# Optimization experiments

Measured on AMD Instinct MI355X. Metric: run time of the kernel, lower is better.

Reference implementation:

```python
import jax, jax.numpy as jnp
import numpy as np
import math

B, L, D, H, FACTOR = 4, 2048, 256, 8, 5
DH = D // H

def setup_inputs() -> dict:
    key = jax.random.key(0)
    ks = jax.random.split(key, 12)
    s = 1.0 / math.sqrt(D)
    return {
        "q": jax.random.normal(ks[0], (B, L, D), jnp.float32),
        "k": jax.random.normal(ks[1], (B, L, D), jnp.float32),
        "v": jax.random.normal(ks[2], (B, L, D), jnp.float32),
        "Wq": jax.random.normal(ks[3], (D, D), jnp.float32) * s,
        "bq": jax.random.normal(ks[4], (D,), jnp.float32) * s,
        "Wk": jax.random.normal(ks[5], (D, D), jnp.float32) * s,
        "bk": jax.random.normal(ks[6], (D,), jnp.float32) * s,
        "Wv": jax.random.normal(ks[7], (D, D), jnp.float32) * s,
        "bv": jax.random.normal(ks[8], (D,), jnp.float32) * s,
        "Wc": jax.random.normal(ks[9], (D, D), jnp.float32) * s,
        "bc": jax.random.normal(ks[10], (D,), jnp.float32) * s,
        "index_sample": jax.random.randint(ks[11], (L,), 0, L),  # U_part = min(5*L*ceil(log1p(L)), L) = L
    }

def reference(q, k, v, Wq, bq, Wk, bk, Wv, bv, Wc, bc, index_sample):
    # projections (torch Linear: x @ W^T + b)
    qp = q @ Wq.T + bq
    kp = k @ Wk.T + bk
    vp = v @ Wv.T + bv
    # NOTE: original reshapes q with a raw view (no transpose), k/v via split()
    q4 = qp.reshape(B, H, L, DH)                       # faithful to q.view(B, H, L, dh)
    k4 = kp.reshape(B, L, H, DH).transpose(0, 2, 1, 3)
    v4 = vp.reshape(B, L, H, DH).transpose(0, 2, 1, 3)
    qf = q4.reshape(B * H, L, DH)
    kf = k4.reshape(B * H, L, DH)
    vf = v4.reshape(B * H, L, DH)
    # random K sampling (with replacement); U_part == L here
    K_sample = kf[:, index_sample, :]                  # [BH, L, dh]
    QK = jnp.einsum('bld,bud->blu', qf, K_sample)      # [BH, L, L]
    M = QK.max(axis=-1) - QK.sum(axis=-1) / L          # sparsity measure [BH, L]
    u = min(FACTOR * math.ceil(math.log1p(L)), L)      # = 40
    _, top_idx = jax.lax.top_k(-M, u)                  # topk(..., largest=False)
    Q_red = jnp.take_along_axis(qf, top_idx[:, :, None], axis=1)  # [BH, u, dh]
    scores = jnp.einsum('bud,bld->bul', Q_red, kf) / math.sqrt(DH)
    probs = jax.nn.softmax(scores, axis=-1)
    out = jnp.einsum('bul,bld->bud', probs, vf)        # [BH, u, dh]
    out = out.reshape(B, H, u, DH).transpose(0, 2, 1, 3).reshape(B, u, D)
    return out @ Wc.T + bc
```

## Files before the change

kernel.cpp:

```cpp
#include <hip/hip_runtime.h>
#include <math.h>

#define B_ 4
#define L_ 2048
#define D_ 256
#define H_ 8
#define DH_ 32
#define NH_ 32
#define U_ 40
#define LD_ 524288
#define NCH_ 16

typedef __attribute__((ext_vector_type(8))) short short8;
typedef __attribute__((ext_vector_type(4))) float floatx4;

static __device__ __forceinline__ unsigned long long ullmin_(unsigned long long a, unsigned long long b) {
    return a < b ? a : b;
}
static __device__ __forceinline__ unsigned short f2bf_rne(float x) {
    unsigned u = __float_as_uint(x);
    unsigned r = u + 0x7FFFu + ((u >> 16) & 1u);
    return (unsigned short)(r >> 16);
}
static __device__ __forceinline__ float bf2f(unsigned short h) {
    return __uint_as_float(((unsigned)h) << 16);
}

__global__ __launch_bounds__(256) void wsplit(const float* __restrict__ Wq,
                                              const float* __restrict__ Wk,
                                              const float* __restrict__ Wv,
                                              unsigned short* __restrict__ Whs,
                                              unsigned short* __restrict__ Wms,
                                              unsigned short* __restrict__ Wls) {
    const int g = blockIdx.x * 256 + threadIdx.x;
    const int mat = g >> 14;
    const int rem = g & 16383;
    const int col = rem >> 6;
    const int k4 = rem & 63;
    const float* W = (mat == 0) ? Wq : (mat == 1) ? Wk : Wv;
    const float4 x = *(const float4*)(W + (size_t)col * 256 + k4 * 4);
    float xs[4] = {x.x, x.y, x.z, x.w};
    unsigned short hv[4], mv[4], lv[4];
#pragma unroll
    for (int j = 0; j < 4; ++j) {
        hv[j] = f2bf_rne(xs[j]);
        const float e1 = xs[j] - bf2f(hv[j]);
        mv[j] = f2bf_rne(e1);
        const float e2 = e1 - bf2f(mv[j]);
        lv[j] = f2bf_rne(e2);
    }
    const int colblk = col >> 6, c64 = col & 63;
    const int nt = c64 >> 4, cin = c64 & 15;
    const int kt = k4 >> 3, kin = (k4 & 7) * 4;
    const size_t o = ((((size_t)mat * 4 + colblk) * 8 + kt) << 11) + nt * 512 + cin * 32 + kin;
    *(ushort4*)(Whs + o) = make_ushort4(hv[0], hv[1], hv[2], hv[3]);
    *(ushort4*)(Wms + o) = make_ushort4(mv[0], mv[1], mv[2], mv[3]);
    *(ushort4*)(Wls + o) = make_ushort4(lv[0], lv[1], lv[2], lv[3]);
}

__global__ __launch_bounds__(256) void gemm_proj(const float* __restrict__ q,
                                                 const float* __restrict__ k,
                                                 const float* __restrict__ v,
                                                 const unsigned short* __restrict__ Whs,
                                                 const unsigned short* __restrict__ Wms,
                                                 const unsigned short* __restrict__ Wls,
                                                 const float* __restrict__ bq,
                                                 const float* __restrict__ bk,
                                                 const float* __restrict__ bv,
                                                 float* __restrict__ qp,
                                                 float* __restrict__ kp,
                                                 float* __restrict__ vp) {
    const int mat = blockIdx.z;
    const float* X = (mat == 0) ? q : (mat == 1) ? k : v;
    const float* bias = (mat == 0) ? bq : (mat == 1) ? bk : bv;
    float* Y = (mat == 0) ? qp : (mat == 1) ? kp : vp;
    const bool vmat = (mat == 2);

    const int t = threadIdx.x;
    const int w = t >> 6, lane = t & 63;
    const int lq = lane & 15, quad = lane >> 4;
    const int rowBase = blockIdx.x * 64 + w * 16;
    const int colBase = blockIdx.y * 128;
    const int fo = lq * 32 + quad * 8;

    floatx4 acc[8];
#pragma unroll
    for (int nt2 = 0; nt2 < 8; ++nt2) acc[nt2] = (floatx4){0.f, 0.f, 0.f, 0.f};

#pragma unroll 2
    for (int kt = 0; kt < 8; ++kt) {
        short8 Ah, Am, Al;
        {
            const float* xr = X + (size_t)(rowBase + lq) * 256 + kt * 32 + quad * 8;
            const float4 x0 = *(const float4*)xr;
            const float4 x1 = *(const float4*)(xr + 4);
            float xs[8] = {x0.x, x0.y, x0.z, x0.w, x1.x, x1.y, x1.z, x1.w};
#pragma unroll
            for (int j = 0; j < 8; ++j) {
                const unsigned short h = f2bf_rne(xs[j]);
                const float e1 = xs[j] - bf2f(h);
                const unsigned short md = f2bf_rne(e1);
                Ah[j] = (short)h;
                Am[j] = (short)md;
                if (!vmat) {
                    const float e2 = e1 - bf2f(md);
                    Al[j] = (short)f2bf_rne(e2);
                }
            }
        }
#pragma unroll
        for (int nt2 = 0; nt2 < 8; ++nt2) {
            const int colblk = (blockIdx.y << 1) | (nt2 >> 2);
            const size_t pb = ((((size_t)mat * 4 + colblk) * 8 + kt) << 11) + (nt2 & 3) * 512 + fo;
            const short8 Bh = *(const short8*)(Whs + pb);
            const short8 Bm = *(const short8*)(Wms + pb);
            floatx4 a = acc[nt2];
            if (!vmat) {
                const short8 Bl = *(const short8*)(Wls + pb);
                a = __builtin_amdgcn_mfma_f32_16x16x32_bf16(Am, Bm, a, 0, 0, 0);
                a = __builtin_amdgcn_mfma_f32_16x16x32_bf16(Ah, Bl, a, 0, 0, 0);
                a = __builtin_amdgcn_mfma_f32_16x16x32_bf16(Al, Bh, a, 0, 0, 0);
                a = __builtin_amdgcn_mfma_f32_16x16x32_bf16(Ah, Bm, a, 0, 0, 0);
                a = __builtin_amdgcn_mfma_f32_16x16x32_bf16(Am, Bh, a, 0, 0, 0);
                a = __builtin_amdgcn_mfma_f32_16x16x32_bf16(Ah, Bh, a, 0, 0, 0);
            } else {
                a = __builtin_amdgcn_mfma_f32_16x16x32_bf16(Ah, Bm, a, 0, 0, 0);
                a = __builtin_amdgcn_mfma_f32_16x16x32_bf16(Am, Bh, a, 0, 0, 0);
                a = __builtin_amdgcn_mfma_f32_16x16x32_bf16(Ah, Bh, a, 0, 0, 0);
            }
            acc[nt2] = a;
        }
    }

#pragma unroll
    for (int nt2 = 0; nt2 < 8; ++nt2) {
        const int c = colBase + nt2 * 16 + lq;
        const float bv_ = bias[c];
#pragma unroll
        for (int r = 0; r < 4; ++r) {
            const int mr = rowBase + quad * 4 + r;
            Y[(size_t)mr * 256 + c] = acc[nt2][r] + bv_;
        }
    }
}

__global__ __launch_bounds__(256) void kconv_ksum(const float* __restrict__ kp,
                                                  const int* __restrict__ idx,
                                                  unsigned short* __restrict__ Khi,
                                                  unsigned short* __restrict__ Klo,
                                                  float* __restrict__ Ksum32) {
    const int blk = blockIdx.x;
    const int i = blk >> 5, uc = blk & 31;
    const int b = i >> 3, h = i & 7;
    const int t = threadIdx.x;
    const int dq = (t & 7) * 4;
    const int ur = t >> 3;

    __shared__ float part[32][36];
    float ksum[4] = {0.f, 0.f, 0.f, 0.f};

#pragma unroll
    for (int p = 0; p < 2; ++p) {
        int u = uc * 64 + p * 32 + ur;
        const float4 x = *(const float4*)(kp + (size_t)b * LD_ + (size_t)idx[u] * D_ + h * DH_ + dq);
        float xs[4] = {x.x, x.y, x.z, x.w};
        unsigned short hv[4], lv[4];
#pragma unroll
        for (int j = 0; j < 4; ++j) {
            ksum[j] += xs[j];
            hv[j] = f2bf_rne(xs[j]);
            lv[j] = f2bf_rne(xs[j] - bf2f(hv[j]));
        }
        size_t o = ((size_t)i * 2048 + u) * 32 + dq;
        *(ushort4*)(Khi + o) = make_ushort4(hv[0], hv[1], hv[2], hv[3]);
        *(ushort4*)(Klo + o) = make_ushort4(lv[0], lv[1], lv[2], lv[3]);
    }
#pragma unroll
    for (int j = 0; j < 4; ++j) part[ur][dq + j] = ksum[j];
    __syncthreads();
    if (t < 32) {
        float s = 0.f;
#pragma unroll 8
        for (int u2 = 0; u2 < 32; ++u2) s += part[u2][t];
        Ksum32[(size_t)blk * 32 + t] = s;
    }
}

__global__ __launch_bounds__(256) void mpart_mfma(const float* __restrict__ qp,
                                                  const unsigned short* __restrict__ Khi,
                                                  const unsigned short* __restrict__ Klo,
                                                  const float* __restrict__ Ksum32,
                                                  float* __restrict__ Mv,
                                                  float* __restrict__ Qmean) {
    const int blk = blockIdx.x;
    const int i = blk >> 5;
    const int lg = blk & 31;
    const int t = threadIdx.x;
    const int w = t >> 6;
    const int lane = t & 63;
    const int lq = lane & 15;
    const int quad = lane >> 4;

    __shared__ float ssum[32];
    __shared__ float red[4][64];
    if (t < 32) {
        float s = 0.f;
#pragma unroll 8
        for (int uc = 0; uc < 32; ++uc) s += Ksum32[((size_t)i * 32 + uc) * 32 + t];
        ssum[t] = s;
    }

    short8 Ah[4], Al[4];
#pragma unroll
    for (int lt = 0; lt < 4; ++lt) {
        const int l = lg * 64 + lt * 16 + lq;
        const float* qrow = qp + ((size_t)i * 2048 + l) * 32 + quad * 8;
        float4 x0 = *(const float4*)(qrow);
        float4 x1 = *(const float4*)(qrow + 4);
        float xs[8] = {x0.x, x0.y, x0.z, x0.w, x1.x, x1.y, x1.z, x1.w};
#pragma unroll
        for (int j = 0; j < 8; ++j) {
            unsigned short h = f2bf_rne(xs[j]);
            unsigned short lo = f2bf_rne(xs[j] - bf2f(h));
            Ah[lt][j] = (short)h;
            Al[lt][j] = (short)lo;
        }
    }

    floatx4 rmax[4];
#pragma unroll
    for (int lt = 0; lt < 4; ++lt)
        rmax[lt] = (floatx4){-INFINITY, -INFINITY, -INFINITY, -INFINITY};

    const size_t kfrag = ((size_t)i * 2048 + w * 512 + lq) * 32 + quad * 8;
    const unsigned short* ph = Khi + kfrag;
    const unsigned short* pl = Klo + kfrag;
#pragma unroll 2
    for (int s = 0; s < 32; ++s) {
        short8 Bh = *(const short8*)(ph + (size_t)s * 512);
        short8 Bl = *(const short8*)(pl + (size_t)s * 512);
#pragma unroll
        for (int lt = 0; lt < 4; ++lt) {
            floatx4 acc = (floatx4){0.f, 0.f, 0.f, 0.f};
            acc = __builtin_amdgcn_mfma_f32_16x16x32_bf16(Al[lt], Bh, acc, 0, 0, 0);
            acc = __builtin_amdgcn_mfma_f32_16x16x32_bf16(Ah[lt], Bl, acc, 0, 0, 0);
            acc = __builtin_amdgcn_mfma_f32_16x16x32_bf16(Ah[lt], Bh, acc, 0, 0, 0);
#pragma unroll
            for (int r = 0; r < 4; ++r) rmax[lt][r] = fmaxf(rmax[lt][r], acc[r]);
        }
    }

#pragma unroll
    for (int lt = 0; lt < 4; ++lt)
#pragma unroll
        for (int r = 0; r < 4; ++r) {
            float v = rmax[lt][r];
#pragma unroll
            for (int off = 1; off < 16; off <<= 1)
                v = fmaxf(v, __shfl_xor(v, off, 64));
            rmax[lt][r] = v;
        }
    if (lq == 0) {
#pragma unroll
        for (int lt = 0; lt < 4; ++lt)
#pragma unroll
            for (int r = 0; r < 4; ++r)
                red[w][lt * 16 + quad * 4 + r] = rmax[lt][r];
    }
    __syncthreads();
    if (t < 64) {
        const int l = lg * 64 + t;
        float m = fmaxf(fmaxf(red[0][t], red[1][t]), fmaxf(red[2][t], red[3][t]));
        const float4* q4 = (const float4*)(qp + ((size_t)i * 2048 + l) * 32);
        const float4* s4 = (const float4*)ssum;
        float qs = 0.f;
#pragma unroll
        for (int z = 0; z < 8; ++z) {
            float4 a = q4[z];
            float4 c = s4[z];
            qs = fmaf(a.x, c.x, qs);
            qs = fmaf(a.y, c.y, qs);
            qs = fmaf(a.z, c.z, qs);
            qs = fmaf(a.w, c.w, qs);
        }
        const float qm = qs * (1.0f / 2048.0f);
        Qmean[(size_t)i * 2048 + l] = qm;
        Mv[(size_t)i * 2048 + l] = m - qm;
    }
}

__global__ __launch_bounds__(256) void topk64_fast(const float* __restrict__ Mv,
                                                   int* __restrict__ candIdx) {
    const int i = blockIdx.x;
    const int t = threadIdx.x;
    const int w = t >> 6, lane = t & 63;

    __shared__ unsigned hist[256];
    __shared__ unsigned sh_prefix, sh_selBelow;
    __shared__ unsigned cnt;
    __shared__ int candLds[64];
    __shared__ unsigned long long wred[4];

    unsigned v[8];
#pragma unroll
    for (int j = 0; j < 8; ++j) {
        const unsigned u = __float_as_uint(Mv[(size_t)i * 2048 + t + 256 * j]);
        v[j] = (u & 0x80000000u) ? ~u : (u | 0x80000000u);
    }

    if (t == 0) { sh_prefix = 0u; sh_selBelow = 0u; cnt = 0u; }

    for (int level = 0; level < 4; ++level) {
        const int shift = 24 - 8 * level;
        __syncthreads();
        const unsigned prefHi = sh_prefix;
        const unsigned selB = sh_selBelow;
        const unsigned mask = (level == 0) ? 0u : (0xFFFFFFFFu << (shift + 8));
        hist[t] = 0u;
        __syncthreads();
#pragma unroll
        for (int j = 0; j < 8; ++j)
            if ((v[j] & mask) == prefHi)
                atomicAdd(&hist[(v[j] >> shift) & 255u], 1u);
        __syncthreads();
        if (t < 64) {
            const unsigned c0 = hist[t * 4 + 0], c1 = hist[t * 4 + 1];
            const unsigned c2 = hist[t * 4 + 2], c3 = hist[t * 4 + 3];
            const unsigned i0 = c0, i1 = c0 + c1, i2 = i1 + c2, i3 = i2 + c3;
            unsigned x = i3;
#pragma unroll
            for (int off = 1; off < 64; off <<= 1) {
                const unsigned y = __shfl_up(x, off, 64);
                if (t >= off) x += y;
            }
            const unsigned excl = x - i3;
            const unsigned r = 64u - selB;
            const unsigned long long ball = __ballot(x >= r);
            const int flane = __ffsll(ball) - 1;
            if (t == flane) {
                unsigned k, ce;
                if (excl + i0 >= r)      { k = 0u; ce = excl; }
                else if (excl + i1 >= r) { k = 1u; ce = excl + i0; }
                else if (excl + i2 >= r) { k = 2u; ce = excl + i1; }
                else                     { k = 3u; ce = excl + i2; }
                sh_prefix = prefHi | (((unsigned)t * 4u + k) << shift);
                sh_selBelow = selB + ce;
            }
        }
    }
    __syncthreads();
    const unsigned thr = sh_prefix;
    const unsigned selB = sh_selBelow;
    const int rem = 64 - (int)selB;

    unsigned long long keys[8];
#pragma unroll
    for (int j = 0; j < 8; ++j) {
        const int l = t + 256 * j;
        if (v[j] < thr) {
            const unsigned p = atomicAdd(&cnt, 1u);
            candLds[p] = l;
            keys[j] = ~0ULL;
        } else if (v[j] == thr) {
            keys[j] = ((unsigned long long)v[j] << 32) | (unsigned)l;
        } else {
            keys[j] = ~0ULL;
        }
    }
    __syncthreads();

    for (int it = 0; it < rem; ++it) {
        unsigned long long best = keys[0];
#pragma unroll
        for (int j = 1; j < 8; ++j) best = ullmin_(best, keys[j]);
#pragma unroll
        for (int off = 1; off < 64; off <<= 1)
            best = ullmin_(best, __shfl_xor(best, off, 64));
        if (lane == 0) wred[w] = best;
        __syncthreads();
        const unsigned long long m = ullmin_(ullmin_(wred[0], wred[1]), ullmin_(wred[2], wred[3]));
        if (t == 0) candLds[selB + it] = (int)(m & 0xffffffffu);
#pragma unroll
        for (int j = 0; j < 8; ++j)
            if (keys[j] == m) keys[j] = ~0ULL;
        __syncthreads();
    }

    if (t < 64) candIdx[i * 64 + t] = candLds[t];
}

__global__ __launch_bounds__(256) void refine_kernel(const float* __restrict__ qp,
                                                     const float* __restrict__ kp,
                                                     const int* __restrict__ idx,
                                                     const int* __restrict__ candIdx,
                                                     float* __restrict__ refPart) {
    const int blk = blockIdx.x;
    const int i = blk >> 3, c = blk & 7;
    const int b = i >> 3, h = i & 7;
    const int t = threadIdx.x;
    __shared__ float qc[64][40];
    __shared__ float Ks[128][40];

    {
        const int cand = t >> 2, dp = (t & 3) * 8;
        const int l = candIdx[i * 64 + cand];
        const float* src = qp + ((size_t)i * 2048 + l) * 32 + dp;
        *(float4*)&qc[cand][dp] = *(const float4*)(src);
        *(float4*)&qc[cand][dp + 4] = *(const float4*)(src + 4);
    }
    __syncthreads();

    const int cand = t >> 2, usub = t & 3;
    float qv[32];
#pragma unroll
    for (int z = 0; z < 8; ++z) {
        float4 a = *(const float4*)&qc[cand][z * 4];
        qv[4 * z] = a.x; qv[4 * z + 1] = a.y; qv[4 * z + 2] = a.z; qv[4 * z + 3] = a.w;
    }

    float m = -INFINITY;
    for (int s = 0; s < 2; ++s) {
        {
            const int r = t >> 1, half = t & 1;
            const int u = c * 256 + s * 128 + r;
            const float* krow = kp + (size_t)b * LD_ + (size_t)idx[u] * D_ + h * DH_ + half * 16;
#pragma unroll
            for (int z = 0; z < 4; ++z)
                *(float4*)&Ks[r][half * 16 + z * 4] = *(const float4*)(krow + z * 4);
        }
        __syncthreads();
        for (int ur = usub; ur < 128; ur += 4) {
            float a0 = 0, a1 = 0, a2 = 0, a3 = 0;
#pragma unroll
            for (int z = 0; z < 8; ++z) {
                float4 kv = *(const float4*)&Ks[ur][z * 4];
                a0 = fmaf(qv[4 * z], kv.x, a0);
                a1 = fmaf(qv[4 * z + 1], kv.y, a1);
                a2 = fmaf(qv[4 * z + 2], kv.z, a2);
                a3 = fmaf(qv[4 * z + 3], kv.w, a3);
            }
            m = fmaxf(m, (a0 + a1) + (a2 + a3));
        }
        __syncthreads();
    }
    m = fmaxf(m, __shfl_xor(m, 1, 64));
    m = fmaxf(m, __shfl_xor(m, 2, 64));
    if ((t & 3) == 0) refPart[((size_t)i * 8 + c) * 64 + cand] = m;
}

#define SCP2 136
#define VSP 36

__global__ __launch_bounds__(320) void attn_part(const float* __restrict__ qp,
                                                 const float* __restrict__ kp,
                                                 const float* __restrict__ vp,
                                                 const int* __restrict__ candIdx,
                                                 const float* __restrict__ refPart,
                                                 const float* __restrict__ Qmean,
                                                 float* __restrict__ mPart,
                                                 float* __restrict__ sPart,
                                                 float* __restrict__ oPart) {
    const int blk = blockIdx.x;
    const int i = blk >> 4, c = blk & 15;
    const int b = i >> 3, h = i & 7;
    const int t = threadIdx.x;

    __shared__ float Qs[40][32];
    __shared__ float Vs[128][VSP];
    __shared__ float sc[40][SCP2];
    __shared__ float mred[40], sred[40];
    __shared__ int topl[40];

    if (t < 64) {
        const int l = candIdx[i * 64 + t];
        float m = -INFINITY;
#pragma unroll
        for (int cc = 0; cc < 8; ++cc) m = fmaxf(m, refPart[((size_t)i * 8 + cc) * 64 + t]);
        float Mex = m - Qmean[(size_t)i * 2048 + l];
        unsigned u32 = __float_as_uint(Mex);
        u32 = (u32 & 0x80000000u) ? ~u32 : (u32 | 0x80000000u);
        unsigned long long key = ((unsigned long long)u32 << 32) | (unsigned)l;
        for (int it = 0; it < 40; ++it) {
            unsigned long long k2 = key;
#pragma unroll
            for (int off = 1; off < 64; off <<= 1) k2 = ullmin_(k2, __shfl_xor(k2, off, 64));
            if (key == k2) {
                topl[it] = l;
                key = ~0ULL;
            }
        }
    } else {
        for (int e = t - 64; e < 1024; e += 256) {
            const int r = e >> 3, qq = e & 7;
            *(float4*)&Vs[r][qq * 4] =
                *(const float4*)(vp + (size_t)b * LD_ + (size_t)(c * 128 + r) * 256 + h * 32 + qq * 4);
        }
    }
    __syncthreads();

    {
        const int r = t >> 3, qq = t & 7;
        const int lq = topl[r];
        *(float4*)&Qs[r][qq * 4] = *(const float4*)(qp + ((size_t)i * 2048 + lq) * 32 + qq * 4);
    }
    __syncthreads();

    const float scale = 0.17677669529663687f;

    if (t < 256) {
        const int r = t >> 1;
        const int j0 = (t & 1) * 20;
        const float* kr = kp + (size_t)b * LD_ + (size_t)(c * 128 + r) * 256 + h * 32;
        float kv[32];
#pragma unroll
        for (int z = 0; z < 8; ++z) {
            float4 x = *(const float4*)(kr + z * 4);
            kv[4 * z] = x.x; kv[4 * z + 1] = x.y; kv[4 * z + 2] = x.z; kv[4 * z + 3] = x.w;
        }
#pragma unroll 4
        for (int jj = 0; jj < 20; ++jj) {
            const int j = j0 + jj;
            float a0 = 0, a1 = 0, a2 = 0, a3 = 0;
#pragma unroll
            for (int z = 0; z < 8; ++z) {
                const float4 q4 = *(const float4*)&Qs[j][z * 4];
                a0 = fmaf(kv[4 * z], q4.x, a0);
                a1 = fmaf(kv[4 * z + 1], q4.y, a1);
                a2 = fmaf(kv[4 * z + 2], q4.z, a2);
                a3 = fmaf(kv[4 * z + 3], q4.w, a3);
            }
            sc[j][r] = ((a0 + a1) + (a2 + a3)) * scale;
        }
    }
    __syncthreads();

    {
        const int w = t >> 6, lane = t & 63;
#pragma unroll
        for (int rr = 0; rr < 8; ++rr) {
            const int j = w * 8 + rr;
            float x0 = sc[j][lane], x1 = sc[j][lane + 64];
            float m = fmaxf(x0, x1);
#pragma unroll
            for (int off = 1; off < 64; off <<= 1) m = fmaxf(m, __shfl_xor(m, off, 64));
            const float e0 = __expf(x0 - m), e1 = __expf(x1 - m);
            sc[j][lane] = e0; sc[j][lane + 64] = e1;
            float s = e0 + e1;
#pragma unroll
            for (int off = 1; off < 64; off <<= 1) s += __shfl_xor(s, off, 64);
            if (lane == 0) { mred[j] = m; sred[j] = s; }
        }
    }
    __syncthreads();

    {
        const int j = t >> 3, qq = t & 7;
        float4 acc = make_float4(0.f, 0.f, 0.f, 0.f);
        for (int l = 0; l < 128; ++l) {
            const float p = sc[j][l];
            const float4 v4 = *(const float4*)&Vs[l][qq * 4];
            acc.x = fmaf(p, v4.x, acc.x);
            acc.y = fmaf(p, v4.y, acc.y);
            acc.z = fmaf(p, v4.z, acc.z);
            acc.w = fmaf(p, v4.w, acc.w);
        }
        const size_t o = (size_t)(i * NCH_ + c) * 40 + j;
        *(float4*)&oPart[o * 32 + qq * 4] = acc;
        if (qq == 0) { mPart[o] = mred[j]; sPart[o] = sred[j]; }
    }
}

__global__ __launch_bounds__(256) void attn_combine(const float* __restrict__ mPart,
                                                    const float* __restrict__ sPart,
                                                    const float* __restrict__ oPart,
                                                    float* __restrict__ attnOut) {
    const int blk = blockIdx.x;
    const int b = blk / 40, j = blk - b * 40;
    const int t = threadIdx.x;
    const int h = t >> 5, d = t & 31;
    const int i = b * 8 + h;

    float mv[NCH_];
    float M = -INFINITY;
#pragma unroll
    for (int c = 0; c < NCH_; ++c) {
        mv[c] = mPart[(size_t)(i * NCH_ + c) * 40 + j];
        M = fmaxf(M, mv[c]);
    }
    float S = 0.f, O = 0.f;
#pragma unroll
    for (int c = 0; c < NCH_; ++c) {
        const float sc_ = __expf(mv[c] - M);
        const size_t o = (size_t)(i * NCH_ + c) * 40 + j;
        S = fmaf(sPart[o], sc_, S);
        O = fmaf(oPart[o * 32 + d], sc_, O);
    }
    attnOut[((size_t)b * 40 + j) * 256 + h * 32 + d] = O / S;
}

__global__ __launch_bounds__(256) void gemm_out(const float* __restrict__ X,
                                                const float* __restrict__ Wc,
                                                const float* __restrict__ bias,
                                                float* __restrict__ Y) {
    const int t = threadIdx.x;
    const int rowBase = blockIdx.x * 16;
    const int colBase = blockIdx.y * 64;
    const int col = colBase + (t & 63);
    const int rq = (t >> 6) * 4;

    __shared__ float Xs[16][256];
#pragma unroll
    for (int e = t; e < 1024; e += 256) {
        const int r = e >> 6, kq = (e & 63) * 4;
        *(float4*)&Xs[r][kq] = *(const float4*)(X + (size_t)(rowBase + r) * 256 + kq);
    }
    __syncthreads();

    const float* wr = Wc + (size_t)col * 256;
    float acc[4] = {0.f, 0.f, 0.f, 0.f};
#pragma unroll 8
    for (int k = 0; k < 256; k += 4) {
        const float4 wv = *(const float4*)(wr + k);
#pragma unroll
        for (int r = 0; r < 4; ++r) {
            acc[r] = fmaf(Xs[rq + r][k + 0], wv.x, acc[r]);
            acc[r] = fmaf(Xs[rq + r][k + 1], wv.y, acc[r]);
            acc[r] = fmaf(Xs[rq + r][k + 2], wv.z, acc[r]);
            acc[r] = fmaf(Xs[rq + r][k + 3], wv.w, acc[r]);
        }
    }

    const float bv = bias[col];
#pragma unroll
    for (int r = 0; r < 4; ++r)
        Y[(size_t)(rowBase + rq + r) * 256 + col] = acc[r] + bv;
}

extern "C" void kernel_launch(void* const* d_in, const int* in_sizes, int n_in,
                              void* d_out, int out_size, void* d_ws, size_t ws_size,
                              hipStream_t stream) {
    const float* q  = (const float*)d_in[0];
    const float* k  = (const float*)d_in[1];
    const float* v  = (const float*)d_in[2];
    const float* Wq = (const float*)d_in[3];
    const float* bq = (const float*)d_in[4];
    const float* Wk = (const float*)d_in[5];
    const float* bk = (const float*)d_in[6];
    const float* Wv = (const float*)d_in[7];
    const float* bv = (const float*)d_in[8];
    const float* Wc = (const float*)d_in[9];
    const float* bc = (const float*)d_in[10];
    const int* idx  = (const int*)d_in[11];
    float* out = (float*)d_out;

    char* w = (char*)d_ws;
    float*          qp      = (float*)(w);
    float*          kp      = (float*)(w + (8u << 20));
    float*          vp      = (float*)(w + (16u << 20));
    unsigned short* Khi     = (unsigned short*)(w + (24u << 20));
    unsigned short* Klo     = (unsigned short*)(w + (28u << 20));
    float*          Mv      = (float*)(w + (32u << 20));
    float*          Qmean   = (float*)(w + (32u << 20) + (256u << 10));
    float*          Ksum32  = (float*)(w + (32u << 20) + (512u << 10));
    int*            candIdx = (int*)  (w + (32u << 20) + (640u << 10));
    float*          refPart = (float*)(w + (32u << 20) + (656u << 10));
    float*          attnOut = (float*)(w + (32u << 20) + (720u << 10));
    unsigned short* Whs     = (unsigned short*)(w + (40u << 20));
    unsigned short* Wms     = (unsigned short*)(w + (40u << 20) + (512u << 10));
    unsigned short* Wls     = (unsigned short*)(w + (41u << 20));
    float*          mPart   = (float*)(w + (24u << 20));
    float*          sPart   = (float*)(w + (24u << 20) + (128u << 10));
    float*          oPart   = (float*)(w + (24u << 20) + (256u << 10));

    hipLaunchKernelGGL(wsplit, dim3(192), dim3(256), 0, stream, Wq, Wk, Wv, Whs, Wms, Wls);
    hipLaunchKernelGGL(gemm_proj, dim3(128, 2, 3), dim3(256), 0, stream,
                       q, k, v, Whs, Wms, Wls, bq, bk, bv, qp, kp, vp);
    hipLaunchKernelGGL(kconv_ksum, dim3(1024), dim3(256), 0, stream, kp, idx, Khi, Klo, Ksum32);
    hipLaunchKernelGGL(mpart_mfma, dim3(1024), dim3(256), 0, stream, qp, Khi, Klo, Ksum32, Mv, Qmean);
    hipLaunchKernelGGL(topk64_fast, dim3(32), dim3(256), 0, stream, Mv, candIdx);
    hipLaunchKernelGGL(refine_kernel, dim3(256), dim3(256), 0, stream, qp, kp, idx, candIdx, refPart);
    hipLaunchKernelGGL(attn_part, dim3(512), dim3(320), 0, stream,
                       qp, kp, vp, candIdx, refPart, Qmean, mPart, sPart, oPart);
    hipLaunchKernelGGL(attn_combine, dim3(160), dim3(256), 0, stream, mPart, sPart, oPart, attnOut);
    hipLaunchKernelGGL(gemm_out, dim3(10, 4), dim3(256), 0, stream, attnOut, Wc, bc, out);
}
```

Before: 227.6 us.

## Stage projection weight tiles in double-buffered LDS shared across waves

The projection GEMM now loads the bf16-split weight tiles once per block into a double-buffered shared-memory array and has all four waves read B fragments from LDS, instead of each wave fetching them from global memory. The next k-tile is prefetched into registers while the current one is consumed, then written to the other buffer. The weight pre-split layout is also permuted so each lane's 8-element fragment is contiguous, which gives coalesced staging loads. This adds 48KB of LDS per block and a barrier per k-step, which may reduce occupancy.

```diff
diff --git a/kernel.cpp b/kernel.cpp
--- a/kernel.cpp
+++ b/kernel.cpp
@@ -50,9 +50,11 @@
         lv[j] = f2bf_rne(e2);
     }
     const int colblk = col >> 6, c64 = col & 63;
-    const int nt = c64 >> 4, cin = c64 & 15;
-    const int kt = k4 >> 3, kin = (k4 & 7) * 4;
-    const size_t o = ((((size_t)mat * 4 + colblk) * 8 + kt) << 11) + nt * 512 + cin * 32 + kin;
+    const int jt = c64 >> 4, cin = c64 & 15;
+    const int kt = k4 >> 3, g8 = k4 & 7;
+    const int quad = g8 >> 1, half = g8 & 1;
+    const size_t o = ((((size_t)mat * 4 + colblk) * 8 + kt) << 11) +
+                     jt * 512 + (quad * 16 + cin) * 8 + half * 4;
     *(ushort4*)(Whs + o) = make_ushort4(hv[0], hv[1], hv[2], hv[3]);
     *(ushort4*)(Wms + o) = make_ushort4(mv[0], mv[1], mv[2], mv[3]);
     *(ushort4*)(Wls + o) = make_ushort4(lv[0], lv[1], lv[2], lv[3]);
@@ -81,14 +83,39 @@
     const int lq = lane & 15, quad = lane >> 4;
     const int rowBase = blockIdx.x * 64 + w * 16;
     const int colBase = blockIdx.y * 128;
-    const int fo = lq * 32 + quad * 8;
+    const int nseg = vmat ? 16 : 24;
+
+    __shared__ unsigned short Bls[2][12288];
 
     floatx4 acc[8];
 #pragma unroll
     for (int nt2 = 0; nt2 < 8; ++nt2) acc[nt2] = (floatx4){0.f, 0.f, 0.f, 0.f};
 
-#pragma unroll 2
+    auto gsrc = [&](int s, int kt) -> const unsigned short* {
+        const int p = s >> 3, rm = s & 7, chunk = rm >> 2, jj = rm & 3;
+        const unsigned short* Wp = (p == 0) ? Whs : (p == 1) ? Wms : Wls;
+        return Wp + (((((size_t)mat * 4 + ((blockIdx.y << 1) | chunk)) * 8 + kt) << 11) +
+                     jj * 512 + lane * 8);
+    };
+
+#pragma unroll
+    for (int n = 0; n < 6; ++n) {
+        const int s = w + n * 4;
+        if (s < nseg)
+            *(short8*)&Bls[0][s * 512 + lane * 8] = *(const short8*)gsrc(s, 0);
+    }
+    __syncthreads();
+
     for (int kt = 0; kt < 8; ++kt) {
+        const int buf = kt & 1;
+
+        short8 stg[6];
+#pragma unroll
+        for (int n = 0; n < 6; ++n) {
+            const int s = w + n * 4;
+            if (kt < 7 && s < nseg) stg[n] = *(const short8*)gsrc(s, kt + 1);
+        }
+
         short8 Ah, Am, Al;
         {
             const float* xr = X + (size_t)(rowBase + lq) * 256 + kt * 32 + quad * 8;
@@ -108,15 +135,16 @@
                 }
             }
         }
+
+        const unsigned short* Bb = Bls[buf];
 #pragma unroll
         for (int nt2 = 0; nt2 < 8; ++nt2) {
-            const int colblk = (blockIdx.y << 1) | (nt2 >> 2);
-            const size_t pb = ((((size_t)mat * 4 + colblk) * 8 + kt) << 11) + (nt2 & 3) * 512 + fo;
-            const short8 Bh = *(const short8*)(Whs + pb);
-            const short8 Bm = *(const short8*)(Wms + pb);
+            const int boff = ((nt2 >> 2) << 11) + ((nt2 & 3) << 9) + lane * 8;
+            const short8 Bh = *(const short8*)&Bb[boff];
+            const short8 Bm = *(const short8*)&Bb[4096 + boff];
             floatx4 a = acc[nt2];
             if (!vmat) {
-                const short8 Bl = *(const short8*)(Wls + pb);
+                const short8 Bl = *(const short8*)&Bb[8192 + boff];
                 a = __builtin_amdgcn_mfma_f32_16x16x32_bf16(Am, Bm, a, 0, 0, 0);
                 a = __builtin_amdgcn_mfma_f32_16x16x32_bf16(Ah, Bl, a, 0, 0, 0);
                 a = __builtin_amdgcn_mfma_f32_16x16x32_bf16(Al, Bh, a, 0, 0, 0);
@@ -130,6 +158,14 @@
             }
             acc[nt2] = a;
         }
+
+#pragma unroll
+        for (int n = 0; n < 6; ++n) {
+            const int s = w + n * 4;
+            if (kt < 7 && s < nseg)
+                *(short8*)&Bls[buf ^ 1][s * 512 + lane * 8] = stg[n];
+        }
+        __syncthreads();
     }
 
 #pragma unroll
```

Result: faster. 210.6 us (-7.5%).
